# Optimization experiments

Hardware: AMD Instinct MI355X
Metric: run time of the kernel (lower is better)

Reference implementation:

```python
import math
import jax, jax.numpy as jnp
import numpy as np

B, L, H = 32, 1024, 128

def setup_inputs() -> dict:
    key = jax.random.key(0)
    k1, k2, k3, k4 = jax.random.split(key, 4)
    a = jax.random.normal(k1, (B, L, H), dtype=jnp.float32)
    b = jax.random.normal(k2, (B, L, H), dtype=jnp.float32)
    mask_a = jax.random.randint(k3, (B, L, 1), 0, 2, dtype=jnp.int32)
    mask_b = jax.random.randint(k4, (B, L, 1), 0, 2, dtype=jnp.int32)
    temperature = jnp.asarray(1.0 / math.sqrt(H), dtype=jnp.float32)
    return {"a": a, "b": b, "mask_a": mask_a, "mask_b": mask_b, "temperature": temperature}

def reference(a, b, mask_a, mask_b, temperature):
    # scores: [B, La, Lb]
    scores = jnp.einsum('bld,bmd->blm', a, b) * temperature
    # outer product of token validity masks -> pair mask [B, La, Lb]
    mask = jnp.einsum('blk,bmk->blm', mask_a.astype(jnp.float32), mask_b.astype(jnp.float32)) > 0
    scores = jnp.where(mask, scores, jnp.float32(-10000.0))
    attention_a = jax.nn.softmax(scores, axis=1)  # normalize over La (columns)
    attention_b = jax.nn.softmax(scores, axis=2)  # normalize over Lb (rows)
    feature_a = jnp.einsum('blm,bmd->bld', attention_b, b)
    feature_b = jnp.einsum('blm,bmd->bld', attention_a, a)  # valid since La == Lb
    return (feature_a, feature_b)
```

## Files before the change

kernel.cpp:

```cpp
#include <hip/hip_runtime.h>
#include <math.h>

#define BN 32
#define LL 1024
#define HH 128

typedef __attribute__((ext_vector_type(8))) short short8;
typedef __attribute__((ext_vector_type(4))) float f32x4;

static const size_t SZ_BF = (size_t)BN * LL * HH * 2;

__device__ __forceinline__ ushort f2bf(float x) {
  union { float f; unsigned u; } c; c.f = x;
  unsigned r = c.u + 0x7fffu + ((c.u >> 16) & 1u);
  return (ushort)(r >> 16);
}
__device__ __forceinline__ float bf2f(ushort h) {
  union { unsigned u; float f; } c; c.u = ((unsigned)h) << 16;
  return c.f;
}
__device__ __forceinline__ short8 ld8(const ushort* p) {
  return *(const short8*)p;
}

__global__ __launch_bounds__(256) void k_convert(
    const float* __restrict__ a, const float* __restrict__ b,
    const int* __restrict__ mask_b,
    ushort* __restrict__ abf, ushort* __restrict__ bbf,
    ushort* __restrict__ aT, ushort* __restrict__ bT,
    float* __restrict__ meanb, float* __restrict__ invmean) {
  int bb = blockIdx.y;
  int l0 = blockIdx.x * 64;
  int which = blockIdx.z;
  const float* src = which ? b : a;
  ushort* dst  = which ? bbf : abf;
  ushort* dstT = which ? bT : aT;
  float* dmean = which ? meanb : invmean;
  __shared__ __align__(16) ushort T[128][72];
  __shared__ float accS[128];
  __shared__ float wgt[64];
  int t = threadIdx.x;
  if (t < 128) accS[t] = 0.f;
  if (t < 64)
    wgt[t] = which ? 1.0f : ((mask_b[bb * LL + l0 + t] == 0) ? 1.0f : 0.0f);
  int lrow = t >> 5;
  int dcol = (t & 31) * 4;
#pragma unroll
  for (int p = 0; p < 8; ++p) {
    int l = p * 8 + lrow;
    float4 v = *(const float4*)&src[((size_t)bb * LL + l0 + l) * HH + dcol];
    ushort4 u;
    u.x = f2bf(v.x); u.y = f2bf(v.y); u.z = f2bf(v.z); u.w = f2bf(v.w);
    *(ushort4*)&dst[((size_t)bb * LL + l0 + l) * HH + dcol] = u;
    T[dcol + 0][l] = u.x; T[dcol + 1][l] = u.y;
    T[dcol + 2][l] = u.z; T[dcol + 3][l] = u.w;
  }
  __syncthreads();
  int drow = t >> 3;
  int c8 = (t & 7) * 8;
#pragma unroll
  for (int q = 0; q < 4; ++q) {
    int d = q * 32 + drow;
    short8 val = *(const short8*)&T[d][c8];
    *(short8*)&dstT[((size_t)bb * HH + d) * LL + l0 + c8] = val;
    float s = 0.f;
#pragma unroll
    for (int j = 0; j < 8; ++j) s += wgt[c8 + j] * bf2f((ushort)val[j]);
    atomicAdd(&accS[d], s);
  }
  __syncthreads();
  if (t < 128) atomicAdd(&dmean[bb * HH + t], accS[t]);
}

__global__ __launch_bounds__(256, 2) void k_colsum(
    const ushort* __restrict__ abf, const ushort* __restrict__ bbf,
    const int* __restrict__ mask_a, const int* __restrict__ mask_b,
    const float* __restrict__ temp_p, float2* __restrict__ cc) {
  int bb = blockIdx.y;
  int m0 = blockIdx.x * 64;
  int t = threadIdx.x;
  int w = t >> 6, lane = t & 63, l16 = lane & 15, quad = lane >> 4;
  float temp = temp_p[0];
  __shared__ float biasA[LL];
  __shared__ float csred[4][4][16];
  for (int i = t; i < LL; i += 256)
    biasA[i] = mask_a[bb * LL + i] ? 0.0f : -10000.0f;

  short8 Bm[4][4];
  float biasB_mt[4];
#pragma unroll
  for (int mt = 0; mt < 4; ++mt) {
    int m = m0 + mt * 16 + l16;
    biasB_mt[mt] = mask_b[bb * LL + m] ? 0.0f : -10000.0f;
#pragma unroll
    for (int k = 0; k < 4; ++k)
      Bm[mt][k] = ld8(&bbf[((size_t)bb * LL + m) * HH + k * 32 + quad * 8]);
  }
  __syncthreads();

  float cs[4] = {0.f, 0.f, 0.f, 0.f};
  for (int it = 0; it < 16; ++it) {
    int lbase = w * 256 + it * 16;
    short8 Al[4];
    const ushort* arow = &abf[((size_t)bb * LL + lbase + l16) * HH];
#pragma unroll
    for (int k = 0; k < 4; ++k) Al[k] = ld8(&arow[k * 32 + quad * 8]);
#pragma unroll
    for (int mt = 0; mt < 4; ++mt) {
      f32x4 sacc = {0.f, 0.f, 0.f, 0.f};
#pragma unroll
      for (int k = 0; k < 4; ++k)
        sacc = __builtin_amdgcn_mfma_f32_16x16x32_bf16(Al[k], Bm[mt][k], sacc, 0, 0, 0);
#pragma unroll
      for (int r = 0; r < 4; ++r) {
        int l = lbase + quad * 4 + r;
        cs[mt] += __expf(sacc[r] * temp + biasA[l] + biasB_mt[mt]);
      }
    }
  }
#pragma unroll
  for (int mt = 0; mt < 4; ++mt) {
    cs[mt] += __shfl_xor(cs[mt], 16);
    cs[mt] += __shfl_xor(cs[mt], 32);
  }
  if (lane < 16) {
#pragma unroll
    for (int mt = 0; mt < 4; ++mt) csred[w][mt][l16] = cs[mt];
  }
  __syncthreads();
  if (t < 64) {
    int mt = t >> 4, ml = t & 15;
    float s = csred[0][mt][ml] + csred[1][mt][ml] + csred[2][mt][ml] + csred[3][mt][ml];
    int m = m0 + t;
    float bB = mask_b[bb * LL + m] ? 0.0f : -10000.0f;
    cc[bb * LL + m] = make_float2(s > 0.f ? 1.0f / s : 0.0f, bB);
  }
}

__global__ __launch_bounds__(256, 2) void k_features(
    const ushort* __restrict__ abf, const ushort* __restrict__ bbf,
    const ushort* __restrict__ aT, const ushort* __restrict__ bT,
    const int* __restrict__ mask_a, const float* __restrict__ temp_p,
    const float2* __restrict__ cc, const float* __restrict__ meanb,
    const float* __restrict__ invmean, float* __restrict__ out) {
  int bb = blockIdx.y;
  int l0 = blockIdx.x * 64;
  int t = threadIdx.x;
  int w = t >> 6, lane = t & 63, l16 = lane & 15, quad = lane >> 4;
  float temp = temp_p[0];

  __shared__ float2 ccs[LL];
  __shared__ __align__(16) ushort Pa[2][64 * 72];
  __shared__ __align__(16) ushort Pb[2][64 * 72];
  __shared__ float rspart[4][64];
  __shared__ float rsfin[64];

  for (int i = t; i < LL; i += 256) ccs[i] = cc[bb * LL + i];

  float biasA_lt[4];
  short8 Afix[4][4];
#pragma unroll
  for (int lt = 0; lt < 4; ++lt) {
    int l = l0 + lt * 16 + l16;
    biasA_lt[lt] = mask_a[bb * LL + l] ? 0.0f : -10000.0f;
#pragma unroll
    for (int k = 0; k < 4; ++k)
      Afix[lt][k] = ld8(&abf[((size_t)bb * LL + l) * HH + k * 32 + quad * 8]);
  }

  f32x4 accA[4][2], accB[4][2];
  f32x4 zero = {0.f, 0.f, 0.f, 0.f};
#pragma unroll
  for (int lt = 0; lt < 4; ++lt)
#pragma unroll
    for (int dt = 0; dt < 2; ++dt) { accA[lt][dt] = zero; accB[lt][dt] = zero; }
  float rs_lt[4] = {0.f, 0.f, 0.f, 0.f};
  __syncthreads();

  int buf = 0;
  for (int m0 = 0; m0 < LL; m0 += 64) {
    short8 Am[4];
    const ushort* brow = &bbf[((size_t)bb * LL + m0 + w * 16 + l16) * HH];
#pragma unroll
    for (int k = 0; k < 4; ++k) Am[k] = ld8(&brow[k * 32 + quad * 8]);
    short8 Bb[2][2], Ba[2][2];
#pragma unroll
    for (int dt = 0; dt < 2; ++dt) {
      const ushort* btrow = &bT[((size_t)bb * HH + w * 32 + dt * 16 + l16) * LL + m0];
      const ushort* atrow = &aT[((size_t)bb * HH + w * 32 + dt * 16 + l16) * LL + m0];
#pragma unroll
      for (int ks = 0; ks < 2; ++ks) {
        Bb[dt][ks] = ld8(&btrow[ks * 32 + quad * 8]);
        Ba[dt][ks] = ld8(&atrow[ks * 32 + quad * 8]);
      }
    }
    float2 cv[4];
#pragma unroll
    for (int r = 0; r < 4; ++r) cv[r] = ccs[m0 + w * 16 + quad * 4 + r];

    ushort* pa = &Pa[buf][0];
    ushort* pb = &Pb[buf][0];
#pragma unroll
    for (int lt = 0; lt < 4; ++lt) {
      f32x4 sacc = zero;
#pragma unroll
      for (int k = 0; k < 4; ++k)
        sacc = __builtin_amdgcn_mfma_f32_16x16x32_bf16(Am[k], Afix[lt][k], sacc, 0, 0, 0);
      ushort pav[4], pbv[4];
#pragma unroll
      for (int r = 0; r < 4; ++r) {
        float e = __expf(sacc[r] * temp + biasA_lt[lt] + cv[r].y);
        pav[r] = f2bf(e);
        rs_lt[lt] += bf2f(pav[r]);
        pbv[r] = f2bf(e * cv[r].x);
      }
      uint2 ka, kb;
      ka.x = (uint)pav[0] | ((uint)pav[1] << 16);
      ka.y = (uint)pav[2] | ((uint)pav[3] << 16);
      kb.x = (uint)pbv[0] | ((uint)pbv[1] << 16);
      kb.y = (uint)pbv[2] | ((uint)pbv[3] << 16);
      int pidx = (lt * 16 + l16) * 72 + w * 16 + quad * 4;
      *(uint2*)&pa[pidx] = ka;
      *(uint2*)&pb[pidx] = kb;
    }
    __syncthreads();

#pragma unroll
    for (int lt = 0; lt < 4; ++lt) {
#pragma unroll
      for (int ks = 0; ks < 2; ++ks) {
        int ridx = (lt * 16 + l16) * 72 + ks * 32 + quad * 8;
        short8 PaF = *(const short8*)&pa[ridx];
        short8 PbF = *(const short8*)&pb[ridx];
#pragma unroll
        for (int dt = 0; dt < 2; ++dt) {
          accA[lt][dt] = __builtin_amdgcn_mfma_f32_16x16x32_bf16(PaF, Bb[dt][ks], accA[lt][dt], 0, 0, 0);
          accB[lt][dt] = __builtin_amdgcn_mfma_f32_16x16x32_bf16(PbF, Ba[dt][ks], accB[lt][dt], 0, 0, 0);
        }
      }
    }
    buf ^= 1;
  }

#pragma unroll
  for (int lt = 0; lt < 4; ++lt) {
    rs_lt[lt] += __shfl_xor(rs_lt[lt], 16);
    rs_lt[lt] += __shfl_xor(rs_lt[lt], 32);
  }
  if (lane < 16) {
#pragma unroll
    for (int lt = 0; lt < 4; ++lt) rspart[w][lt * 16 + l16] = rs_lt[lt];
  }
  __syncthreads();
  if (t < 64)
    rsfin[t] = rspart[0][t] + rspart[1][t] + rspart[2][t] + rspart[3][t];
  __syncthreads();

  float* outA = out;
  float* outB = out + (size_t)BN * LL * HH;
#pragma unroll
  for (int dt = 0; dt < 2; ++dt) {
    int d = w * 32 + dt * 16 + l16;
    float mb = meanb[bb * HH + d] * (1.0f / 1024.0f);
    float im = invmean[bb * HH + d] * (1.0f / 1024.0f);
#pragma unroll
    for (int lt = 0; lt < 4; ++lt) {
#pragma unroll
      for (int r = 0; r < 4; ++r) {
        int l = lt * 16 + quad * 4 + r;
        float rsv = rsfin[l];
        float fa = (rsv > 0.f) ? accA[lt][dt][r] / rsv : mb;
        float fb = accB[lt][dt][r] + im;
        outA[((size_t)bb * LL + l0 + l) * HH + d] = fa;
        outB[((size_t)bb * LL + l0 + l) * HH + d] = fb;
      }
    }
  }
}

extern "C" void kernel_launch(void* const* d_in, const int* in_sizes, int n_in,
                              void* d_out, int out_size, void* d_ws, size_t ws_size,
                              hipStream_t stream) {
  const float* a = (const float*)d_in[0];
  const float* b = (const float*)d_in[1];
  const int* mask_a = (const int*)d_in[2];
  const int* mask_b = (const int*)d_in[3];
  const float* temp = (const float*)d_in[4];
  float* out = (float*)d_out;

  char* wsb = (char*)d_ws;
  ushort* abf = (ushort*)(wsb + 0 * SZ_BF);
  ushort* bbf = (ushort*)(wsb + 1 * SZ_BF);
  ushort* aT  = (ushort*)(wsb + 2 * SZ_BF);
  ushort* bT  = (ushort*)(wsb + 3 * SZ_BF);
  float2* cc  = (float2*)(wsb + 4 * SZ_BF);
  float* meanb   = (float*)(wsb + 4 * SZ_BF + (size_t)BN * LL * sizeof(float2));
  float* invmean = meanb + BN * HH;

  hipMemsetAsync(meanb, 0, 2 * BN * HH * sizeof(float), stream);
  k_convert<<<dim3(16, 32, 2), 256, 0, stream>>>(a, b, mask_b, abf, bbf, aT, bT,
                                                 meanb, invmean);
  k_colsum<<<dim3(16, 32), 256, 0, stream>>>(abf, bbf, mask_a, mask_b, temp, cc);
  k_features<<<dim3(16, 32), 256, 0, stream>>>(abf, bbf, aT, bT, mask_a, temp,
                                               cc, meanb, invmean, out);
  (void)in_sizes; (void)n_in; (void)out_size; (void)ws_size;
}
```

Baseline: 181.6 us.

## Fold column-softmax scale into transposed A, share one P tile, halve tiles

A new k_scale kernel multiplies the transposed bf16 A by the per-column inverse softmax sums. k_features can then reuse the single unnormalised probability tile for both output GEMMs instead of building a second scaled P tile. Row sums are now taken with an MFMA against a ones vector, which replaces the shuffle and shared-memory reduction. Tiles shrink from 64 to 32 rows in colsum and features, doubling the grid and raising the occupancy bounds. The cost is an extra kernel launch plus a read-modify-write pass over aT, and bf16 rounding now happens at a different point.

```diff
diff --git a/kernel.cpp b/kernel.cpp
--- a/kernel.cpp
+++ b/kernel.cpp
@@ -72,33 +72,33 @@
   if (t < 128) atomicAdd(&dmean[bb * HH + t], accS[t]);
 }
 
-__global__ __launch_bounds__(256, 2) void k_colsum(
+__global__ __launch_bounds__(256, 4) void k_colsum(
     const ushort* __restrict__ abf, const ushort* __restrict__ bbf,
     const int* __restrict__ mask_a, const int* __restrict__ mask_b,
-    const float* __restrict__ temp_p, float2* __restrict__ cc) {
+    const float* __restrict__ temp_p, float* __restrict__ invc) {
   int bb = blockIdx.y;
-  int m0 = blockIdx.x * 64;
+  int m0 = blockIdx.x * 32;
   int t = threadIdx.x;
   int w = t >> 6, lane = t & 63, l16 = lane & 15, quad = lane >> 4;
   float temp = temp_p[0];
   __shared__ float biasA[LL];
-  __shared__ float csred[4][4][16];
+  __shared__ float csred[4][2][16];
   for (int i = t; i < LL; i += 256)
     biasA[i] = mask_a[bb * LL + i] ? 0.0f : -10000.0f;
 
-  short8 Bm[4][4];
-  float biasB_mt[4];
-#pragma unroll
-  for (int mt = 0; mt < 4; ++mt) {
+  short8 Bm[2][4];
+  float biasB[2];
+#pragma unroll
+  for (int mt = 0; mt < 2; ++mt) {
     int m = m0 + mt * 16 + l16;
-    biasB_mt[mt] = mask_b[bb * LL + m] ? 0.0f : -10000.0f;
+    biasB[mt] = mask_b[bb * LL + m] ? 0.0f : -10000.0f;
 #pragma unroll
     for (int k = 0; k < 4; ++k)
       Bm[mt][k] = ld8(&bbf[((size_t)bb * LL + m) * HH + k * 32 + quad * 8]);
   }
   __syncthreads();
 
-  float cs[4] = {0.f, 0.f, 0.f, 0.f};
+  float cs[2] = {0.f, 0.f};
   for (int it = 0; it < 16; ++it) {
     int lbase = w * 256 + it * 16;
     short8 Al[4];
@@ -106,7 +106,7 @@
 #pragma unroll
     for (int k = 0; k < 4; ++k) Al[k] = ld8(&arow[k * 32 + quad * 8]);
 #pragma unroll
-    for (int mt = 0; mt < 4; ++mt) {
+    for (int mt = 0; mt < 2; ++mt) {
       f32x4 sacc = {0.f, 0.f, 0.f, 0.f};
 #pragma unroll
       for (int k = 0; k < 4; ++k)
@@ -114,67 +114,87 @@
 #pragma unroll
       for (int r = 0; r < 4; ++r) {
         int l = lbase + quad * 4 + r;
-        cs[mt] += __expf(sacc[r] * temp + biasA[l] + biasB_mt[mt]);
+        cs[mt] += __expf(sacc[r] * temp + biasA[l] + biasB[mt]);
       }
     }
   }
 #pragma unroll
-  for (int mt = 0; mt < 4; ++mt) {
+  for (int mt = 0; mt < 2; ++mt) {
     cs[mt] += __shfl_xor(cs[mt], 16);
     cs[mt] += __shfl_xor(cs[mt], 32);
   }
   if (lane < 16) {
 #pragma unroll
-    for (int mt = 0; mt < 4; ++mt) csred[w][mt][l16] = cs[mt];
-  }
-  __syncthreads();
-  if (t < 64) {
-    int mt = t >> 4, ml = t & 15;
-    float s = csred[0][mt][ml] + csred[1][mt][ml] + csred[2][mt][ml] + csred[3][mt][ml];
-    int m = m0 + t;
-    float bB = mask_b[bb * LL + m] ? 0.0f : -10000.0f;
-    cc[bb * LL + m] = make_float2(s > 0.f ? 1.0f / s : 0.0f, bB);
-  }
-}
-
-__global__ __launch_bounds__(256, 2) void k_features(
+    for (int mt = 0; mt < 2; ++mt) csred[w][mt][l16] = cs[mt];
+  }
+  __syncthreads();
+  if (t < 32) {
+    float s = csred[0][t >> 4][t & 15] + csred[1][t >> 4][t & 15] +
+              csred[2][t >> 4][t & 15] + csred[3][t >> 4][t & 15];
+    invc[bb * LL + m0 + t] = s > 0.f ? 1.0f / s : 0.0f;
+  }
+}
+
+__global__ __launch_bounds__(256) void k_scale(
+    ushort* __restrict__ aT, const float* __restrict__ invc) {
+  size_t base = ((size_t)blockIdx.x * 256 + threadIdx.x) * 8;
+  int b = (int)(base >> 17);
+  int m = (int)(base & (LL - 1));
+  short8 v = *(short8*)&aT[base];
+  float4 i0 = *(const float4*)&invc[b * LL + m];
+  float4 i1 = *(const float4*)&invc[b * LL + m + 4];
+  short8 o;
+  o[0] = (short)f2bf(bf2f((ushort)v[0]) * i0.x);
+  o[1] = (short)f2bf(bf2f((ushort)v[1]) * i0.y);
+  o[2] = (short)f2bf(bf2f((ushort)v[2]) * i0.z);
+  o[3] = (short)f2bf(bf2f((ushort)v[3]) * i0.w);
+  o[4] = (short)f2bf(bf2f((ushort)v[4]) * i1.x);
+  o[5] = (short)f2bf(bf2f((ushort)v[5]) * i1.y);
+  o[6] = (short)f2bf(bf2f((ushort)v[6]) * i1.z);
+  o[7] = (short)f2bf(bf2f((ushort)v[7]) * i1.w);
+  *(short8*)&aT[base] = o;
+}
+
+__global__ __launch_bounds__(256, 3) void k_features(
     const ushort* __restrict__ abf, const ushort* __restrict__ bbf,
-    const ushort* __restrict__ aT, const ushort* __restrict__ bT,
-    const int* __restrict__ mask_a, const float* __restrict__ temp_p,
-    const float2* __restrict__ cc, const float* __restrict__ meanb,
+    const ushort* __restrict__ aS, const ushort* __restrict__ bT,
+    const int* __restrict__ mask_a, const int* __restrict__ mask_b,
+    const float* __restrict__ temp_p, const float* __restrict__ meanb,
     const float* __restrict__ invmean, float* __restrict__ out) {
   int bb = blockIdx.y;
-  int l0 = blockIdx.x * 64;
+  int l0 = blockIdx.x * 32;
   int t = threadIdx.x;
   int w = t >> 6, lane = t & 63, l16 = lane & 15, quad = lane >> 4;
   float temp = temp_p[0];
 
-  __shared__ float2 ccs[LL];
-  __shared__ __align__(16) ushort Pa[2][64 * 72];
-  __shared__ __align__(16) ushort Pb[2][64 * 72];
-  __shared__ float rspart[4][64];
-  __shared__ float rsfin[64];
-
-  for (int i = t; i < LL; i += 256) ccs[i] = cc[bb * LL + i];
-
-  float biasA_lt[4];
-  short8 Afix[4][4];
-#pragma unroll
-  for (int lt = 0; lt < 4; ++lt) {
+  __shared__ float biasBs[LL];
+  __shared__ __align__(16) ushort Pa[2][32 * 72];
+
+  for (int i = t; i < LL; i += 256)
+    biasBs[i] = mask_b[bb * LL + i] ? 0.0f : -10000.0f;
+
+  float biasA_lt[2];
+  short8 Afix[2][4];
+#pragma unroll
+  for (int lt = 0; lt < 2; ++lt) {
     int l = l0 + lt * 16 + l16;
     biasA_lt[lt] = mask_a[bb * LL + l] ? 0.0f : -10000.0f;
 #pragma unroll
     for (int k = 0; k < 4; ++k)
       Afix[lt][k] = ld8(&abf[((size_t)bb * LL + l) * HH + k * 32 + quad * 8]);
   }
-
-  f32x4 accA[4][2], accB[4][2];
+  short8 Bones;
+#pragma unroll
+  for (int j = 0; j < 8; ++j) Bones[j] = (short)0x3F80;
+
+  f32x4 accA[2][2], accB[2][2], accR[2];
   f32x4 zero = {0.f, 0.f, 0.f, 0.f};
 #pragma unroll
-  for (int lt = 0; lt < 4; ++lt)
+  for (int lt = 0; lt < 2; ++lt) {
+    accR[lt] = zero;
 #pragma unroll
     for (int dt = 0; dt < 2; ++dt) { accA[lt][dt] = zero; accB[lt][dt] = zero; }
-  float rs_lt[4] = {0.f, 0.f, 0.f, 0.f};
+  }
   __syncthreads();
 
   int buf = 0;
@@ -183,78 +203,55 @@
     const ushort* brow = &bbf[((size_t)bb * LL + m0 + w * 16 + l16) * HH];
 #pragma unroll
     for (int k = 0; k < 4; ++k) Am[k] = ld8(&brow[k * 32 + quad * 8]);
-    short8 Bb[2][2], Ba[2][2];
+    short8 Bb[2][2], Bs[2][2];
 #pragma unroll
     for (int dt = 0; dt < 2; ++dt) {
-      const ushort* btrow = &bT[((size_t)bb * HH + w * 32 + dt * 16 + l16) * LL + m0];
-      const ushort* atrow = &aT[((size_t)bb * HH + w * 32 + dt * 16 + l16) * LL + m0];
+      size_t drow = (size_t)bb * HH + w * 32 + dt * 16 + l16;
+      const ushort* btrow = &bT[drow * LL + m0];
+      const ushort* asrow = &aS[drow * LL + m0];
 #pragma unroll
       for (int ks = 0; ks < 2; ++ks) {
         Bb[dt][ks] = ld8(&btrow[ks * 32 + quad * 8]);
-        Ba[dt][ks] = ld8(&atrow[ks * 32 + quad * 8]);
+        Bs[dt][ks] = ld8(&asrow[ks * 32 + quad * 8]);
       }
     }
-    float2 cv[4];
-#pragma unroll
-    for (int r = 0; r < 4; ++r) cv[r] = ccs[m0 + w * 16 + quad * 4 + r];
+    float bB[4];
+#pragma unroll
+    for (int r = 0; r < 4; ++r) bB[r] = biasBs[m0 + w * 16 + quad * 4 + r];
 
     ushort* pa = &Pa[buf][0];
-    ushort* pb = &Pb[buf][0];
-#pragma unroll
-    for (int lt = 0; lt < 4; ++lt) {
+#pragma unroll
+    for (int lt = 0; lt < 2; ++lt) {
       f32x4 sacc = zero;
 #pragma unroll
       for (int k = 0; k < 4; ++k)
         sacc = __builtin_amdgcn_mfma_f32_16x16x32_bf16(Am[k], Afix[lt][k], sacc, 0, 0, 0);
-      ushort pav[4], pbv[4];
-#pragma unroll
-      for (int r = 0; r < 4; ++r) {
-        float e = __expf(sacc[r] * temp + biasA_lt[lt] + cv[r].y);
-        pav[r] = f2bf(e);
-        rs_lt[lt] += bf2f(pav[r]);
-        pbv[r] = f2bf(e * cv[r].x);
-      }
-      uint2 ka, kb;
+      ushort pav[4];
+#pragma unroll
+      for (int r = 0; r < 4; ++r)
+        pav[r] = f2bf(__expf(sacc[r] * temp + biasA_lt[lt] + bB[r]));
+      uint2 ka;
       ka.x = (uint)pav[0] | ((uint)pav[1] << 16);
       ka.y = (uint)pav[2] | ((uint)pav[3] << 16);
-      kb.x = (uint)pbv[0] | ((uint)pbv[1] << 16);
-      kb.y = (uint)pbv[2] | ((uint)pbv[3] << 16);
-      int pidx = (lt * 16 + l16) * 72 + w * 16 + quad * 4;
-      *(uint2*)&pa[pidx] = ka;
-      *(uint2*)&pb[pidx] = kb;
+      *(uint2*)&pa[(lt * 16 + l16) * 72 + w * 16 + quad * 4] = ka;
     }
     __syncthreads();
 
 #pragma unroll
-    for (int lt = 0; lt < 4; ++lt) {
+    for (int lt = 0; lt < 2; ++lt) {
 #pragma unroll
       for (int ks = 0; ks < 2; ++ks) {
-        int ridx = (lt * 16 + l16) * 72 + ks * 32 + quad * 8;
-        short8 PaF = *(const short8*)&pa[ridx];
-        short8 PbF = *(const short8*)&pb[ridx];
+        short8 PaF = *(const short8*)&pa[(lt * 16 + l16) * 72 + ks * 32 + quad * 8];
+        accR[lt] = __builtin_amdgcn_mfma_f32_16x16x32_bf16(PaF, Bones, accR[lt], 0, 0, 0);
 #pragma unroll
         for (int dt = 0; dt < 2; ++dt) {
           accA[lt][dt] = __builtin_amdgcn_mfma_f32_16x16x32_bf16(PaF, Bb[dt][ks], accA[lt][dt], 0, 0, 0);
-          accB[lt][dt] = __builtin_amdgcn_mfma_f32_16x16x32_bf16(PbF, Ba[dt][ks], accB[lt][dt], 0, 0, 0);
+          accB[lt][dt] = __builtin_amdgcn_mfma_f32_16x16x32_bf16(PaF, Bs[dt][ks], accB[lt][dt], 0, 0, 0);
         }
       }
     }
     buf ^= 1;
   }
-
-#pragma unroll
-  for (int lt = 0; lt < 4; ++lt) {
-    rs_lt[lt] += __shfl_xor(rs_lt[lt], 16);
-    rs_lt[lt] += __shfl_xor(rs_lt[lt], 32);
-  }
-  if (lane < 16) {
-#pragma unroll
-    for (int lt = 0; lt < 4; ++lt) rspart[w][lt * 16 + l16] = rs_lt[lt];
-  }
-  __syncthreads();
-  if (t < 64)
-    rsfin[t] = rspart[0][t] + rspart[1][t] + rspart[2][t] + rspart[3][t];
-  __syncthreads();
 
   float* outA = out;
   float* outB = out + (size_t)BN * LL * HH;
@@ -264,15 +261,15 @@
     float mb = meanb[bb * HH + d] * (1.0f / 1024.0f);
     float im = invmean[bb * HH + d] * (1.0f / 1024.0f);
 #pragma unroll
-    for (int lt = 0; lt < 4; ++lt) {
+    for (int lt = 0; lt < 2; ++lt) {
 #pragma unroll
       for (int r = 0; r < 4; ++r) {
-        int l = lt * 16 + quad * 4 + r;
-        float rsv = rsfin[l];
+        int l = l0 + lt * 16 + quad * 4 + r;
+        float rsv = accR[lt][r];
         float fa = (rsv > 0.f) ? accA[lt][dt][r] / rsv : mb;
         float fb = accB[lt][dt][r] + im;
-        outA[((size_t)bb * LL + l0 + l) * HH + d] = fa;
-        outB[((size_t)bb * LL + l0 + l) * HH + d] = fb;
+        outA[((size_t)bb * LL + l) * HH + d] = fa;
+        outB[((size_t)bb * LL + l) * HH + d] = fb;
       }
     }
   }
@@ -293,15 +290,16 @@
   ushort* bbf = (ushort*)(wsb + 1 * SZ_BF);
   ushort* aT  = (ushort*)(wsb + 2 * SZ_BF);
   ushort* bT  = (ushort*)(wsb + 3 * SZ_BF);
-  float2* cc  = (float2*)(wsb + 4 * SZ_BF);
-  float* meanb   = (float*)(wsb + 4 * SZ_BF + (size_t)BN * LL * sizeof(float2));
+  float* invc = (float*)(wsb + 4 * SZ_BF);
+  float* meanb   = invc + (size_t)BN * LL;
   float* invmean = meanb + BN * HH;
 
   hipMemsetAsync(meanb, 0, 2 * BN * HH * sizeof(float), stream);
   k_convert<<<dim3(16, 32, 2), 256, 0, stream>>>(a, b, mask_b, abf, bbf, aT, bT,
                                                  meanb, invmean);
-  k_colsum<<<dim3(16, 32), 256, 0, stream>>>(abf, bbf, mask_a, mask_b, temp, cc);
-  k_features<<<dim3(16, 32), 256, 0, stream>>>(abf, bbf, aT, bT, mask_a, temp,
-                                               cc, meanb, invmean, out);
+  k_colsum<<<dim3(32, 32), 256, 0, stream>>>(abf, bbf, mask_a, mask_b, temp, invc);
+  k_scale<<<dim3(2048), 256, 0, stream>>>(aT, invc);
+  k_features<<<dim3(32, 32), 256, 0, stream>>>(abf, bbf, aT, bT, mask_a, mask_b,
+                                               temp, meanb, invmean, out);
   (void)in_sizes; (void)n_in; (void)out_size; (void)ws_size;
 }
```

After: 236.0 us. 1.3x slower.
